# Performance work log

Hardware: AMD Instinct MI355X
Metric: run time of the kernel (lower is better)

## Reference

```python
import jax, jax.numpy as jnp
import numpy as np

COMMITMENT_COST = 0.25
NUM_EMBEDDINGS = 512
EMBEDDING_DIM = 64


def setup_inputs() -> dict:
    key = jax.random.key(0)
    k1, k2 = jax.random.split(key)
    inputs = jax.random.normal(k1, (32, EMBEDDING_DIM, 64, 64), dtype=jnp.float32)  # NCHW
    embedding_weight = jax.random.normal(k2, (NUM_EMBEDDINGS, EMBEDDING_DIM), dtype=jnp.float32)
    return {"inputs": inputs, "embedding_weight": embedding_weight}


def reference(inputs, embedding_weight):
    # NCHW -> NHWC, flatten to [N, D]
    x = jnp.transpose(inputs, (0, 2, 3, 1))  # [B,H,W,D]
    input_shape = x.shape
    flat = x.reshape(-1, EMBEDDING_DIM)  # [N, D]

    distances = (jnp.sum(flat * flat, axis=1, keepdims=True)
                 + jnp.sum(embedding_weight * embedding_weight, axis=1)
                 - 2.0 * jnp.matmul(flat, embedding_weight.T))

    encoding_indices = jnp.argmin(distances, axis=1)  # [N]
    encodings = jax.nn.one_hot(encoding_indices, NUM_EMBEDDINGS, dtype=jnp.float32)  # [N, K]

    # quantized lookup (== encodings @ embedding_weight)
    quantized = jnp.take(embedding_weight, encoding_indices, axis=0).reshape(input_shape)

    # commitment loss (eval path; EMA buffer updates are a training-time side effect)
    encoder_loss = jnp.mean((jax.lax.stop_gradient(quantized) - x) ** 2)
    loss = COMMITMENT_COST * encoder_loss

    # straight-through estimator
    quantized_st = x + jax.lax.stop_gradient(quantized - x)

    avg_probs = jnp.mean(encodings, axis=0)
    perplexity = jnp.exp(-jnp.sum(avg_probs * jnp.log(avg_probs + 1e-10)))

    return (loss, jnp.transpose(quantized_st, (0, 3, 1, 2)), perplexity, encodings)
```

## Files before the change

### kernel.cpp

```cpp
#include <hip/hip_runtime.h>
#include <math.h>

#define N_ROWS 131072
#define D 64
#define K 512
#define BLK 512
#define ROWS_PER_BLK 512
#define GRID (N_ROWS / ROWS_PER_BLK)
#define MARGIN 4e-3f


typedef __attribute__((ext_vector_type(8))) _Float16 f16x8;
typedef __attribute__((ext_vector_type(4))) float    f32x4;

#define MFMA(a, b, c) __builtin_amdgcn_mfma_f32_16x16x32_f16((a), (b), (c), 0, 0, 0)

#define OFF_EH   0
#define OFF_EL   65536
#define OFF_XH   0
#define OFF_XL   65536
#define OFF_E2   131072
#define OFF_IDX  133120
#define OFF_REF  135168
#define ARENA_SZ 137216

__device__ __forceinline__ unsigned pk2(_Float16 a, _Float16 b) {
    return (unsigned)__builtin_bit_cast(unsigned short, a) |
           ((unsigned)__builtin_bit_cast(unsigned short, b) << 16);
}

#define CT_ALL(M) M(0) M(1) M(2) M(3)
#define UPD(rt, s, ki) { \
    bool lt1 = (s) < s1_##rt; bool lt2 = (s) < s2_##rt; \
    s2_##rt = lt1 ? s1_##rt : (lt2 ? (s) : s2_##rt); \
    i2_##rt = lt1 ? i1_##rt : (lt2 ? (ki) : i2_##rt); \
    s1_##rt = lt1 ? (s) : s1_##rt; \
    i1_##rt = lt1 ? (ki) : i1_##rt; }

__device__ __forceinline__ void dist_pass(
    const char* ebase, const float* e2L, int fq, int fr,
    f16x8 xh0_0, f16x8 xh0_1, f16x8 xl0_0, f16x8 xl0_1,
    f16x8 xh1_0, f16x8 xh1_1, f16x8 xl1_0, f16x8 xl1_1,
    int* s_idxL, int* s_refL, int row0)
{
    float s1_0 = INFINITY, s2_0 = INFINITY, s1_1 = INFINITY, s2_1 = INFINITY;
    int   i1_0 = 0, i2_0 = 0, i1_1 = 0, i2_1 = 0;

    for (int cb = 0; cb < 8; ++cb) {
        const int cbBase = cb * 64 + fq * 4;

#define LDE2(ct) f32x4 e2q##ct = *(const f32x4*)(e2L + cb * 64 + ct * 16 + fq * 4);
        CT_ALL(LDE2)
#undef LDE2

#define LDE(ct) \
        const int c##ct = cb * 64 + ct * 16 + fr; \
        const char* rb##ct = ebase + c##ct * 128; \
        const unsigned xr##ct = (unsigned)((c##ct & 7) << 4); \
        f16x8 eh##ct##_0 = *(const f16x8*)(rb##ct + OFF_EH + (((unsigned)(fq*16 +  0)) ^ xr##ct)); \
        f16x8 eh##ct##_1 = *(const f16x8*)(rb##ct + OFF_EH + (((unsigned)(fq*16 + 64)) ^ xr##ct)); \
        f16x8 el##ct##_0 = *(const f16x8*)(rb##ct + OFF_EL + (((unsigned)(fq*16 +  0)) ^ xr##ct)); \
        f16x8 el##ct##_1 = *(const f16x8*)(rb##ct + OFF_EL + (((unsigned)(fq*16 + 64)) ^ xr##ct));
        CT_ALL(LDE)
#undef LDE

#define ACC1(rt, ct) \
        f32x4 a##rt##_##ct = {0.f, 0.f, 0.f, 0.f}; \
        a##rt##_##ct = MFMA(eh##ct##_0, xh##rt##_0, a##rt##_##ct); \
        a##rt##_##ct = MFMA(eh##ct##_1, xh##rt##_1, a##rt##_##ct); \
        a##rt##_##ct = MFMA(el##ct##_0, xh##rt##_0, a##rt##_##ct); \
        a##rt##_##ct = MFMA(el##ct##_1, xh##rt##_1, a##rt##_##ct); \
        a##rt##_##ct = MFMA(eh##ct##_0, xl##rt##_0, a##rt##_##ct); \
        a##rt##_##ct = MFMA(eh##ct##_1, xl##rt##_1, a##rt##_##ct);
#define ACC_CT(ct) ACC1(0, ct) ACC1(1, ct)
        CT_ALL(ACC_CT)
#undef ACC_CT
#undef ACC1

#define SCJ(rt, ct, j) { \
        float s = fmaf(-2.f, a##rt##_##ct[j], e2q##ct[j]); \
        int ki = cbBase + ct * 16 + j; \
        UPD(rt, s, ki) }
#define SC4(rt, ct) SCJ(rt, ct, 0) SCJ(rt, ct, 1) SCJ(rt, ct, 2) SCJ(rt, ct, 3)
#define SC_CT(ct) SC4(0, ct) SC4(1, ct)
        CT_ALL(SC_CT)
#undef SC_CT
#undef SC4
#undef SCJ
    }

#define MERGE(rt, off) { \
    float b1 = __shfl_xor(s1_##rt, off); int bi1 = __shfl_xor(i1_##rt, off); \
    float b2 = __shfl_xor(s2_##rt, off); int bi2 = __shfl_xor(i2_##rt, off); \
    bool bf = (b1 < s1_##rt) || (b1 == s1_##rt && bi1 < i1_##rt); \
    float c1 = bf ? b1 : s1_##rt; int ci1 = bf ? bi1 : i1_##rt; \
    float lw = bf ? s1_##rt : b1; int lwi = bf ? i1_##rt : bi1; \
    float d2 = bf ? b2 : s2_##rt; int di2 = bf ? bi2 : i2_##rt; \
    bool ds = (d2 < lw) || (d2 == lw && di2 < lwi); \
    s1_##rt = c1; i1_##rt = ci1; \
    s2_##rt = ds ? d2 : lw; i2_##rt = ds ? di2 : lwi; }
    MERGE(0, 16) MERGE(0, 32) MERGE(1, 16) MERGE(1, 32)
#undef MERGE

    if (fq == 0) {
        s_idxL[row0 + fr] = i1_0;
        s_refL[row0 + fr] = (s2_0 - s1_0 < MARGIN) ? i2_0 : -1;
        s_idxL[row0 + fr + 16] = i1_1;
        s_refL[row0 + fr + 16] = (s2_1 - s1_1 < MARGIN) ? i2_1 : -1;
    }
}

__global__ __launch_bounds__(BLK, 2) void vq_dist_kernel(
    const float* __restrict__ in,
    const float* __restrict__ emb,
    float* __restrict__ enc_out)
{
    __shared__ __align__(16) char s_arena[ARENA_SZ];
    float* e2L    = (float*)(s_arena + OFF_E2);
    int*   s_idxL = (int*)(s_arena + OFF_IDX);
    int*   s_refL = (int*)(s_arena + OFF_REF);

    const int tid  = threadIdx.x;
    const int lane = tid & 63;
    const int w    = tid >> 6;
    const int fr   = lane & 15;
    const int fq   = lane >> 4;

    {
        const int nn = blockIdx.x * ROWS_PER_BLK + tid;
        const int bb = nn >> 12, hww = nn & 4095;
        const float* xp = in + (size_t)bb * 262144 + hww;
        char* xhW = s_arena + OFF_XH;
        char* xlW = s_arena + OFF_XL;
        const unsigned rbase = (unsigned)tid * 128u;
        const unsigned rxor  = (unsigned)((tid & 7) << 4);
        #pragma unroll
        for (int i = 0; i < 64; i += 2) {
            float f0 = xp[i * 4096];
            float f1 = xp[(i + 1) * 4096];
            _Float16 h0 = (_Float16)f0; _Float16 l0 = (_Float16)(f0 - (float)h0);
            _Float16 h1 = (_Float16)f1; _Float16 l1 = (_Float16)(f1 - (float)h1);
            unsigned off = rbase + (((unsigned)(i * 2)) ^ rxor);
            *(unsigned*)(xhW + off) = pk2(h0, h1);
            *(unsigned*)(xlW + off) = pk2(l0, l1);
        }
    }
    __syncthreads();

    const char* xb = s_arena;
    const int xr0 = w * 64 + fr;
#define LDX1(t, half) \
    *(const f16x8*)(xb + OFF_XH + (unsigned)(xr0 + t * 16) * 128u + \
        (((unsigned)(fq * 16 + half * 64)) ^ ((unsigned)(((xr0 + t * 16) & 7) << 4))))
#define LDX1L(t, half) \
    *(const f16x8*)(xb + OFF_XL + (unsigned)(xr0 + t * 16) * 128u + \
        (((unsigned)(fq * 16 + half * 64)) ^ ((unsigned)(((xr0 + t * 16) & 7) << 4))))
#define LDXF(t) \
    f16x8 xh##t##_0 = LDX1(t, 0); \
    f16x8 xh##t##_1 = LDX1(t, 1); \
    f16x8 xl##t##_0 = LDX1L(t, 0); \
    f16x8 xl##t##_1 = LDX1L(t, 1);
    LDXF(0) LDXF(1) LDXF(2) LDXF(3)
#undef LDXF
#undef LDX1
#undef LDX1L
    __syncthreads();

    {
        char* eb = s_arena;
        #pragma unroll
        for (int it = 0; it < 16; ++it) {
            int j = tid + it * 512;
            int c = j >> 4, q = j & 15;
            float4 e = ((const float4*)emb)[j];
            _Float16 h0 = (_Float16)e.x; _Float16 l0 = (_Float16)(e.x - (float)h0);
            _Float16 h1 = (_Float16)e.y; _Float16 l1 = (_Float16)(e.y - (float)h1);
            _Float16 h2 = (_Float16)e.z; _Float16 l2 = (_Float16)(e.z - (float)h2);
            _Float16 h3 = (_Float16)e.w; _Float16 l3 = (_Float16)(e.w - (float)h3);
            unsigned xr = (unsigned)((c & 7) << 4);
            unsigned base = (unsigned)(c * 128) + (((unsigned)(q * 8)) ^ xr);
            *(uint2*)(eb + OFF_EH + base) = make_uint2(pk2(h0, h1), pk2(h2, h3));
            *(uint2*)(eb + OFF_EL + base) = make_uint2(pk2(l0, l1), pk2(l2, l3));

            float p = e.x * e.x;
            p = fmaf(e.y, e.y, p);
            p = fmaf(e.z, e.z, p);
            p = fmaf(e.w, e.w, p);
            p += __shfl_xor(p, 1);
            p += __shfl_xor(p, 2);
            p += __shfl_xor(p, 4);
            p += __shfl_xor(p, 8);
            if (q == 0) e2L[c] = p;
        }
    }
    __syncthreads();

    dist_pass(s_arena, e2L, fq, fr,
              xh0_0, xh0_1, xl0_0, xl0_1, xh1_0, xh1_1, xl1_0, xl1_1,
              s_idxL, s_refL, w * 64);
    dist_pass(s_arena, e2L, fq, fr,
              xh2_0, xh2_1, xl2_0, xl2_1, xh3_0, xh3_1, xl3_0, xl3_1,
              s_idxL, s_refL, w * 64 + 32);

    {
        const int n = blockIdx.x * ROWS_PER_BLK + tid;
        int i1 = s_idxL[tid];
        int ir = s_refL[tid];
        *(int*)(enc_out + (size_t)n * K) = i1 | ((ir + 1) << 16);
    }
}

__global__ __launch_bounds__(256) void vq_out_kernel(
    const float* __restrict__ in,
    const float* __restrict__ emb,
    unsigned int* __restrict__ counts,
    unsigned long long* __restrict__ loss_acc,
    float* __restrict__ quant_out,
    float* __restrict__ enc)
{
    __shared__ unsigned int s_hist[K];
    __shared__ int s_idx[256];
    __shared__ double s_red[256];
    const int tid = threadIdx.x;
    const int n = blockIdx.x * 256 + tid;
    s_hist[tid] = 0u; s_hist[tid + 256] = 0u;
    __syncthreads();

    const int b = n >> 12, hw = n & 4095;
    const float* xin = in + (size_t)b * 262144 + hw;
    const int packed = *(const int*)(enc + (size_t)n * K);
    int i1 = packed & 0xFFFF;
    const int ir = (packed >> 16) - 1;
    if (ir >= 0) {
        double dA = 0.0, dB = 0.0;
        const float* eA = emb + i1 * D;
        const float* eB = emb + ir * D;
        for (int d = 0; d < D; ++d) {
            double xv = (double)xin[d * 4096];
            double tA = xv - (double)eA[d]; dA = fma(tA, tA, dA);
            double tB = xv - (double)eB[d]; dB = fma(tB, tB, dB);
        }
        if (dB < dA || (dB == dA && ir < i1)) i1 = ir;
    }
    s_idx[tid] = i1;
    atomicAdd(&s_hist[i1], 1u);

    const float4* eq = (const float4*)(emb + (size_t)i1 * D);
    float* qout = quant_out + (size_t)b * 262144 + hw;
    float lsum = 0.f;
    #pragma unroll
    for (int i = 0; i < 16; ++i) {
        float4 q = eq[i];
        float x0 = xin[(4 * i + 0) * 4096], x1 = xin[(4 * i + 1) * 4096];
        float x2 = xin[(4 * i + 2) * 4096], x3 = xin[(4 * i + 3) * 4096];
        float d0 = q.x - x0; lsum = fmaf(d0, d0, lsum);
        float d1 = q.y - x1; lsum = fmaf(d1, d1, lsum);
        float d2 = q.z - x2; lsum = fmaf(d2, d2, lsum);
        float d3 = q.w - x3; lsum = fmaf(d3, d3, lsum);
        __builtin_nontemporal_store(q.x, &qout[(4 * i + 0) * 4096]);
        __builtin_nontemporal_store(q.y, &qout[(4 * i + 1) * 4096]);
        __builtin_nontemporal_store(q.z, &qout[(4 * i + 2) * 4096]);
        __builtin_nontemporal_store(q.w, &qout[(4 * i + 3) * 4096]);
    }
    s_red[tid] = (double)lsum;
    __syncthreads();

    {
        const int wv   = tid >> 6;
        const int lane = tid & 63;
        const int r0   = wv * 64;
        float* brow = enc + ((size_t)blockIdx.x * 256 + r0) * K;
        const int c0 = lane * 4;
        #pragma unroll 8
        for (int i = 0; i < 64; ++i) {
            const int idx = s_idx[r0 + i];
            float* rp = brow + (size_t)i * K;
            f32x4 v0, v1;
            v0.x = (c0 + 0 == idx) ? 1.f : 0.f;
            v0.y = (c0 + 1 == idx) ? 1.f : 0.f;
            v0.z = (c0 + 2 == idx) ? 1.f : 0.f;
            v0.w = (c0 + 3 == idx) ? 1.f : 0.f;
            v1.x = (256 + c0 + 0 == idx) ? 1.f : 0.f;
            v1.y = (256 + c0 + 1 == idx) ? 1.f : 0.f;
            v1.z = (256 + c0 + 2 == idx) ? 1.f : 0.f;
            v1.w = (256 + c0 + 3 == idx) ? 1.f : 0.f;
            __builtin_nontemporal_store(v0, (f32x4*)(rp + c0));
            __builtin_nontemporal_store(v1, (f32x4*)(rp + 256 + c0));
        }
    }

    __syncthreads();
    for (int s = 128; s > 0; s >>= 1) {
        if (tid < s) s_red[tid] += s_red[tid + s];
        __syncthreads();
    }
    if (tid == 0) {
        unsigned long long q =
            (unsigned long long)(long long)llrint(s_red[0] * 1073741824.0);
        atomicAdd(loss_acc, q);
    }
    {
        unsigned int c0h = s_hist[tid];
        if (c0h) atomicAdd(&counts[tid], c0h);
        unsigned int c1h = s_hist[tid + 256];
        if (c1h) atomicAdd(&counts[tid + 256], c1h);
    }
}

__global__ __launch_bounds__(512) void vq_final_kernel(
    const unsigned int* __restrict__ counts,
    const unsigned long long* __restrict__ loss_acc,
    float* __restrict__ out_loss,
    float* __restrict__ out_perp)
{
    __shared__ double sp[512];
    int t = threadIdx.x;
    double p = (double)counts[t] / (double)N_ROWS;
    sp[t] = p * log(p + 1e-10);
    __syncthreads();
    for (int s = 256; s > 0; s >>= 1) {
        if (t < s) sp[t] += sp[t + s];
        __syncthreads();
    }
    if (t == 0) {
        double ls = (double)(long long)(*loss_acc) * (1.0 / 1073741824.0);
        *out_loss = (float)(0.25 * ls / 8388608.0);
        *out_perp = (float)exp(-sp[0]);
    }
}

extern "C" void kernel_launch(void* const* d_in, const int* in_sizes, int n_in,
                              void* d_out, int out_size, void* d_ws, size_t ws_size,
                              hipStream_t stream) {
    const float* in  = (const float*)d_in[0];
    const float* emb = (const float*)d_in[1];
    float* out = (float*)d_out;

    unsigned int* counts = (unsigned int*)d_ws;
    unsigned long long* loss_acc = (unsigned long long*)((char*)d_ws + 2048);

    hipMemsetAsync(d_ws, 0, 2056, stream);
    vq_dist_kernel<<<GRID, BLK, 0, stream>>>(in, emb, out + 8388610);
    vq_out_kernel<<<N_ROWS / 256, 256, 0, stream>>>(in, emb, counts, loss_acc,
                                                    out + 1, out + 8388610);
    vq_final_kernel<<<1, 512, 0, stream>>>(counts, loss_acc, out, out + 8388609);
}
```

Baseline: 135.4 us.

## Move fp64 refinement into dist kernel and split one-hot writes into separate blocks

The near-tie fp64 refinement now runs at the end of the distance kernel, which writes the final index both into the one-hot buffer and into the quantized output slot as a handoff. The output kernel's grid is split 4:1: four of every five blocks only write one-hot rows (16 rows per wave, loading indices straight from global), and the fifth does the quantized gather, loss and histogram. The aim is to spread the large encodings store across more independent blocks and drop the shared-memory index staging and a barrier. The cost is an extra scattered store and reload through the quantized output for the index handoff.

```diff
diff --git a/kernel.cpp b/kernel.cpp
--- a/kernel.cpp
+++ b/kernel.cpp
@@ -113,6 +113,7 @@
 __global__ __launch_bounds__(BLK, 2) void vq_dist_kernel(
     const float* __restrict__ in,
     const float* __restrict__ emb,
+    float* __restrict__ quant_out,
     float* __restrict__ enc_out)
 {
     __shared__ __align__(16) char s_arena[ARENA_SZ];
@@ -204,9 +205,24 @@
 
     {
         const int n = blockIdx.x * ROWS_PER_BLK + tid;
+        const int b = n >> 12, hw = n & 4095;
         int i1 = s_idxL[tid];
-        int ir = s_refL[tid];
-        *(int*)(enc_out + (size_t)n * K) = i1 | ((ir + 1) << 16);
+        const int ir = s_refL[tid];
+        if (ir >= 0) {
+            const float* xin = in + (size_t)b * 262144 + hw;
+            double dA = 0.0, dB = 0.0;
+            const float* eA = emb + i1 * D;
+            const float* eB = emb + ir * D;
+            for (int d = 0; d < D; ++d) {
+                double xv = (double)xin[d * 4096];
+                double tA = xv - (double)eA[d]; dA = fma(tA, tA, dA);
+                double tB = xv - (double)eB[d]; dB = fma(tB, tB, dB);
+            }
+            if (dB < dA || (dB == dA && ir < i1)) i1 = ir;
+        }
+        const float fbits = __int_as_float(i1);
+        enc_out[(size_t)n * K] = fbits;
+        quant_out[(size_t)b * 262144 + hw] = fbits;
     }
 }
 
@@ -219,30 +235,49 @@
     float* __restrict__ enc)
 {
     __shared__ unsigned int s_hist[K];
-    __shared__ int s_idx[256];
     __shared__ double s_red[256];
     const int tid = threadIdx.x;
-    const int n = blockIdx.x * 256 + tid;
+    const int grp = blockIdx.x / 5;
+    const int sub = blockIdx.x % 5;
+
+    if (sub < 4) {
+        const int eb   = grp * 4 + sub;
+        const int wv   = tid >> 6;
+        const int lane = tid & 63;
+        const size_t row0 = (size_t)eb * 64 + (size_t)wv * 16;
+
+        int idxs[16];
+        #pragma unroll
+        for (int i = 0; i < 16; ++i)
+            idxs[i] = __float_as_int(enc[(row0 + i) * K]);
+
+        const int c0 = lane * 4;
+        #pragma unroll
+        for (int i = 0; i < 16; ++i) {
+            const int idx = idxs[i];
+            float* rp = enc + (row0 + i) * K;
+            f32x4 v0, v1;
+            v0.x = (c0 + 0 == idx) ? 1.f : 0.f;
+            v0.y = (c0 + 1 == idx) ? 1.f : 0.f;
+            v0.z = (c0 + 2 == idx) ? 1.f : 0.f;
+            v0.w = (c0 + 3 == idx) ? 1.f : 0.f;
+            v1.x = (256 + c0 + 0 == idx) ? 1.f : 0.f;
+            v1.y = (256 + c0 + 1 == idx) ? 1.f : 0.f;
+            v1.z = (256 + c0 + 2 == idx) ? 1.f : 0.f;
+            v1.w = (256 + c0 + 3 == idx) ? 1.f : 0.f;
+            __builtin_nontemporal_store(v0, (f32x4*)(rp + c0));
+            __builtin_nontemporal_store(v1, (f32x4*)(rp + 256 + c0));
+        }
+        return;
+    }
+
+    const int n = grp * 256 + tid;
     s_hist[tid] = 0u; s_hist[tid + 256] = 0u;
     __syncthreads();
 
     const int b = n >> 12, hw = n & 4095;
     const float* xin = in + (size_t)b * 262144 + hw;
-    const int packed = *(const int*)(enc + (size_t)n * K);
-    int i1 = packed & 0xFFFF;
-    const int ir = (packed >> 16) - 1;
-    if (ir >= 0) {
-        double dA = 0.0, dB = 0.0;
-        const float* eA = emb + i1 * D;
-        const float* eB = emb + ir * D;
-        for (int d = 0; d < D; ++d) {
-            double xv = (double)xin[d * 4096];
-            double tA = xv - (double)eA[d]; dA = fma(tA, tA, dA);
-            double tB = xv - (double)eB[d]; dB = fma(tB, tB, dB);
-        }
-        if (dB < dA || (dB == dA && ir < i1)) i1 = ir;
-    }
-    s_idx[tid] = i1;
+    const int i1 = __float_as_int(quant_out[(size_t)b * 262144 + hw]);
     atomicAdd(&s_hist[i1], 1u);
 
     const float4* eq = (const float4*)(emb + (size_t)i1 * D);
@@ -262,33 +297,8 @@
         __builtin_nontemporal_store(q.z, &qout[(4 * i + 2) * 4096]);
         __builtin_nontemporal_store(q.w, &qout[(4 * i + 3) * 4096]);
     }
+
     s_red[tid] = (double)lsum;
-    __syncthreads();
-
-    {
-        const int wv   = tid >> 6;
-        const int lane = tid & 63;
-        const int r0   = wv * 64;
-        float* brow = enc + ((size_t)blockIdx.x * 256 + r0) * K;
-        const int c0 = lane * 4;
-        #pragma unroll 8
-        for (int i = 0; i < 64; ++i) {
-            const int idx = s_idx[r0 + i];
-            float* rp = brow + (size_t)i * K;
-            f32x4 v0, v1;
-            v0.x = (c0 + 0 == idx) ? 1.f : 0.f;
-            v0.y = (c0 + 1 == idx) ? 1.f : 0.f;
-            v0.z = (c0 + 2 == idx) ? 1.f : 0.f;
-            v0.w = (c0 + 3 == idx) ? 1.f : 0.f;
-            v1.x = (256 + c0 + 0 == idx) ? 1.f : 0.f;
-            v1.y = (256 + c0 + 1 == idx) ? 1.f : 0.f;
-            v1.z = (256 + c0 + 2 == idx) ? 1.f : 0.f;
-            v1.w = (256 + c0 + 3 == idx) ? 1.f : 0.f;
-            __builtin_nontemporal_store(v0, (f32x4*)(rp + c0));
-            __builtin_nontemporal_store(v1, (f32x4*)(rp + 256 + c0));
-        }
-    }
-
     __syncthreads();
     for (int s = 128; s > 0; s >>= 1) {
         if (tid < s) s_red[tid] += s_red[tid + s];
@@ -340,8 +350,8 @@
     unsigned long long* loss_acc = (unsigned long long*)((char*)d_ws + 2048);
 
     hipMemsetAsync(d_ws, 0, 2056, stream);
-    vq_dist_kernel<<<GRID, BLK, 0, stream>>>(in, emb, out + 8388610);
-    vq_out_kernel<<<N_ROWS / 256, 256, 0, stream>>>(in, emb, counts, loss_acc,
-                                                    out + 1, out + 8388610);
+    vq_dist_kernel<<<GRID, BLK, 0, stream>>>(in, emb, out + 1, out + 8388610);
+    vq_out_kernel<<<2560, 256, 0, stream>>>(in, emb, counts, loss_acc,
+                                            out + 1, out + 8388610);
     vq_final_kernel<<<1, 512, 0, stream>>>(counts, loss_acc, out, out + 8388609);
 }
```

Result: faster. 125.3 us (-7.5%).
